# Kernel tuning notes

Measured on AMD Instinct MI355X. Metric: run time of the kernel, lower is better.

## Reference

```python
import jax, jax.numpy as jnp
import numpy as np

B, N, F, H, K, C = 2048, 62, 512, 128, 2, 2
EPS_BN = 1e-5
EPS_NORM = 1e-10
N_TRIL = N * (N + 1) // 2  # 1953, tril_indices incl. diagonal
FC_SIZES = [H * N, H * N // 2, H * N // 4, H * N // 8, C]  # [7936,3968,1984,992,2]


def setup_inputs() -> dict:
    key = jax.random.key(0)
    ks = jax.random.split(key, 16)
    inp = {
        "x": jax.random.normal(ks[0], (B, N, F), jnp.float32),
        "edge_weight": jax.random.uniform(ks[1], (N_TRIL,), jnp.float32),
        "bn_gamma": jnp.ones((F,), jnp.float32),
        "bn_beta": jnp.zeros((F,), jnp.float32),
        # xavier_normal for SGConv lin
        "lin_w": jax.random.normal(ks[2], (H, F), jnp.float32) * (2.0 / (F + H)) ** 0.5,
        "lin_b": jnp.zeros((H,), jnp.float32),
    }
    for i in range(4):
        fan_in, fan_out = FC_SIZES[i], FC_SIZES[i + 1]
        inp[f"fc{i}_w"] = jax.random.normal(ks[3 + i], (fan_out, fan_in), jnp.float32) * (2.0 / (fan_in + fan_out)) ** 0.5
        inp[f"fc{i}_b"] = jnp.zeros((fan_out,), jnp.float32)
    return inp


def _normalized_adj(edge_weight):
    """Build symmetric dense adjacency from tril params, normalize_matrix
    (relu + sym deg-norm), then SGConv.norm (D^-1/2 A D^-1/2; self-loops are
    already on the diagonal so add_remaining_self_loops is a no-op)."""
    xs, ys = np.tril_indices(N)
    Wm = jnp.zeros((N, N), jnp.float32).at[xs, ys].set(edge_weight)
    Wm = Wm + Wm.T - jnp.diag(jnp.diag(Wm))
    A = jax.nn.relu(Wm)
    dinv = jax.lax.rsqrt(A.sum(1) + EPS_NORM)
    A = dinv[:, None] * A * dinv[None, :]
    # SGConv normalization: deg = scatter_add over rows -> row sums
    deg = A.sum(1)
    dis = jnp.where(deg > 0, deg ** -0.5, 0.0)
    return dis[:, None] * A * dis[None, :]


def reference(x, edge_weight, bn_gamma, bn_beta, lin_w, lin_b,
              fc0_w, fc0_b, fc1_w, fc1_b, fc2_w, fc2_b, fc3_w, fc3_b):
    A = _normalized_adj(edge_weight)  # [N, N], shared across batch
    # BatchNorm1d over feature channels, stats over (batch, node) dims (train mode)
    mean = x.mean((0, 1))
    var = x.var((0, 1))
    h = (x - mean) * jax.lax.rsqrt(var + EPS_BN) * bn_gamma + bn_beta  # [B,N,F]
    # K-hop SGConv propagation == dense matmul with shared normalized adjacency
    for _ in range(K):
        h = jnp.einsum('ij,bjf->bif', A, h)
    h = h @ lin_w.T + lin_b           # [B, N, H]
    h = h.reshape(B, N * H)           # node-major flatten, matches x.view(batch,-1)
    # dropout is identity in eval mode
    for W, b in ((fc0_w, fc0_b), (fc1_w, fc1_b), (fc2_w, fc2_b)):
        h = jax.nn.relu(h @ W.T + b)
    return h @ fc3_w.T + fc3_b        # [B, C]
```

## Files before the change

kernel.cpp:

```cpp
#include <hip/hip_runtime.h>

typedef _Float16 f16;
typedef __attribute__((ext_vector_type(4))) _Float16 f16x4;
typedef __attribute__((ext_vector_type(8))) _Float16 f16x8;
typedef __attribute__((ext_vector_type(4))) float f32x4;

#define DEVI static __device__ __forceinline__

DEVI void async_copy16(const f16* g, f16* l) {
  __builtin_amdgcn_global_load_lds(
      (const __attribute__((address_space(1))) void*)g,
      (__attribute__((address_space(3))) void*)l, 16, 0, 0);
}

#define MEMPIN asm volatile("" ::: "memory")
#define RBAR __builtin_amdgcn_s_barrier()

__global__ __launch_bounds__(1024) void k_adj(const float* __restrict__ ew, float* __restrict__ out)
{
  __shared__ float sW[62][64];
  __shared__ float sT[62][64];
  __shared__ float d[62];
  const int tid = threadIdx.x;
  for (int idx = tid; idx < 62 * 62; idx += 1024) {
    int i = idx / 62, j = idx % 62;
    float w = (j <= i) ? ew[i * (i + 1) / 2 + j] : ew[j * (j + 1) / 2 + i];
    sW[i][j] = fmaxf(w, 0.f);
  }
  __syncthreads();
  if (tid < 62) {
    float s = 0.f;
    for (int j = 0; j < 62; j++) s += sW[tid][j];
    d[tid] = rsqrtf(s + 1e-10f);
  }
  __syncthreads();
  for (int idx = tid; idx < 62 * 62; idx += 1024) {
    int i = idx / 62, j = idx % 62;
    sW[i][j] *= d[i] * d[j];
  }
  __syncthreads();
  if (tid < 62) {
    float s = 0.f;
    for (int j = 0; j < 62; j++) s += sW[tid][j];
    d[tid] = (s > 0.f) ? rsqrtf(s) : 0.f;
  }
  __syncthreads();
  for (int idx = tid; idx < 62 * 62; idx += 1024) {
    int i = idx / 62, j = idx % 62;
    sW[i][j] *= d[i] * d[j];
  }
  __syncthreads();
  for (int idx = tid; idx < 62 * 64; idx += 1024) {
    int i = idx >> 6, j = idx & 63;
    float s = 0.f;
    if (j < 62) {
      for (int k = 0; k < 62; k++) s += sW[i][k] * sW[k][j];
    }
    sT[i][j] = s;
    out[idx] = s;
  }
  __syncthreads();
  if (tid < 62) {
    float s = 0.f;
    for (int j = 0; j < 62; j++) s += sT[tid][j];
    out[62 * 64 + tid] = s;
  }
}

__global__ __launch_bounds__(1024) void k_bnstats(const float* __restrict__ X, float* __restrict__ part)
{
  const int tid = threadIdx.x;
  const int c4 = (tid & 127) << 2;
  const int rg = tid >> 7;
  float sx = 0, sy = 0, sz = 0, sw = 0, qx = 0, qy = 0, qz = 0, qw = 0;
  const long r0 = (long)blockIdx.x * 496 + rg;
  for (int i = 0; i < 62; i++) {
    const float4 v = *(const float4*)(X + (r0 + 8 * i) * 512 + c4);
    sx += v.x; sy += v.y; sz += v.z; sw += v.w;
    qx += v.x * v.x; qy += v.y * v.y; qz += v.z * v.z; qw += v.w * v.w;
  }
  __shared__ float red[1024][8];
  red[tid][0] = sx; red[tid][1] = sy; red[tid][2] = sz; red[tid][3] = sw;
  red[tid][4] = qx; red[tid][5] = qy; red[tid][6] = qz; red[tid][7] = qw;
  __syncthreads();
  if (tid < 128) {
    float acc8[8];
#pragma unroll
    for (int j = 0; j < 8; j++) acc8[j] = 0.f;
#pragma unroll
    for (int g = 0; g < 8; g++)
#pragma unroll
      for (int j = 0; j < 8; j++) acc8[j] += red[g * 128 + tid][j];
    float* p = part + (long)blockIdx.x * 1024;
#pragma unroll
    for (int j = 0; j < 4; j++) p[c4 + j] = acc8[j];
#pragma unroll
    for (int j = 0; j < 4; j++) p[512 + c4 + j] = acc8[4 + j];
  }
}

__global__ __launch_bounds__(512) void k_bnfin(const float* __restrict__ part, const float* __restrict__ g,
                                               const float* __restrict__ be, float* __restrict__ ssb)
{
  const int c = threadIdx.x;
  float s = 0.f, q = 0.f;
  for (int b = 0; b < 256; b++) {
    s += part[b * 1024 + c];
    q += part[b * 1024 + 512 + c];
  }
  const float inv = 1.f / 126976.f;
  const float mean = s * inv;
  const float var = q * inv - mean * mean;
  const float sc = g[c] * rsqrtf(var + 1e-5f);
  ssb[c] = sc;
  ssb[512 + c] = be[c] - mean * sc;
}

__global__ __launch_bounds__(256) void k_foldw1(const float* __restrict__ lw, const float* __restrict__ ssb,
                                                f16* __restrict__ w1h, float* __restrict__ b1p)
{
  const int h = blockIdx.x;
  const int tid = threadIdx.x;
  float partl = 0.f;
  for (int f = tid; f < 512; f += 256) {
    const float w = lw[h * 512 + f];
    w1h[h * 512 + f] = (f16)(w * ssb[f]);
    partl += w * ssb[512 + f];
  }
  __shared__ float red[256];
  red[tid] = partl;
  __syncthreads();
  for (int s = 128; s; s >>= 1) {
    if (tid < s) red[tid] += red[tid + s];
    __syncthreads();
  }
  if (tid == 0) b1p[h] = red[0];
}

__global__ __launch_bounds__(256) void k_cvtw(const float* __restrict__ src, f16* __restrict__ dst,
                                              int N, int K, int Npad, int Kpad)
{
  const long total4 = (long)Npad * Kpad / 4;
  const int kp4 = Kpad >> 2;
  for (long i = (long)blockIdx.x * 256 + threadIdx.x; i < total4; i += (long)gridDim.x * 256) {
    const long n = i / kp4;
    const int k = (int)(i % kp4) << 2;
    f16x4 h;
    if (n < N && k < K) {
      const float4 v = *(const float4*)(src + n * K + k);
      h[0] = (f16)v.x; h[1] = (f16)v.y; h[2] = (f16)v.z; h[3] = (f16)v.w;
    } else {
      h[0] = (f16)0.f; h[1] = (f16)0.f; h[2] = (f16)0.f; h[3] = (f16)0.f;
    }
    *(f16x4*)(dst + i * 4) = h;
  }
}

__global__ __launch_bounds__(256, 2) void k_linprop(
    const float* __restrict__ X, const f16* __restrict__ Bw,
    const float* __restrict__ A2, const float* __restrict__ b1p,
    const float* __restrict__ lb, f16* __restrict__ Z)
{
  __shared__ f16 smem[128 * 128];
  __shared__ float sA2[62 * 64];
  __shared__ float sR[62];
  __shared__ float sB1[128];
  __shared__ float sLB[128];
  f16* sA = smem;
  f16* sB = smem + 8192;
  const int tid = threadIdx.x;
  const int lane = tid & 63;
  const int wave = tid >> 6;
  const int wr = wave >> 1, wc = wave & 1;
  const long rowA0 = (long)blockIdx.x * 124;

  for (int i = tid; i < 992; i += 256)
    *(float4*)&sA2[i * 4] = *(const float4*)(A2 + i * 4);
  if (tid < 62) sR[tid] = A2[3968 + tid];
  if (tid < 128) sB1[tid] = b1p[tid];
  if (tid >= 128) sLB[tid - 128] = lb[tid - 128];

  const int srow = tid >> 3;
  const int scolb = (tid & 7) << 4;
  const int gcolb = scolb ^ ((srow & 7) << 4);
  const f16* gB = Bw + (long)srow * 512 + (gcolb >> 1);
  f16* lB = sB + srow * 64 + (scolb >> 1);

  const int ac4 = tid & 15;
  const int ar0 = tid >> 4;
  const int aswz = (ar0 & 7) << 4;
  char* lAbase = (char*)sA + ar0 * 128 + ((ac4 * 8) ^ aswz);

  const int frow = lane & 15;
  const int kb = (lane >> 4) << 4;
  const int rswz = (lane & 7) << 4;

  f32x4 acc[4][4] = {};

  for (int kt = 0; kt < 512; kt += 64) {
#pragma unroll
    for (int i = 0; i < 8; i++) {
      long rr = rowA0 + ar0 + 16 * i;
      if (rr > 126975) rr = 126975;
      const float4 v = *(const float4*)(X + rr * 512 + kt + ac4 * 4);
      f16x4 hh;
      hh[0] = (f16)v.x; hh[1] = (f16)v.y; hh[2] = (f16)v.z; hh[3] = (f16)v.w;
      *(f16x4*)(lAbase + 16 * i * 128) = hh;
    }
#pragma unroll
    for (int i = 0; i < 4; i++)
      async_copy16(gB + kt + (long)i * (32 * 512), lB + i * 2048);
    __syncthreads();
#pragma unroll
    for (int kk = 0; kk < 2; kk++) {
      f16x8 af[4], bf[4];
#pragma unroll
      for (int m = 0; m < 4; m++) {
        const int row = wr * 64 + m * 16 + frow;
        af[m] = *(const f16x8*)((const char*)sA + row * 128 + ((kk * 64 + kb) ^ rswz));
      }
#pragma unroll
      for (int n = 0; n < 4; n++) {
        const int row = wc * 64 + n * 16 + frow;
        bf[n] = *(const f16x8*)((const char*)sB + row * 128 + ((kk * 64 + kb) ^ rswz));
      }
#pragma unroll
      for (int m = 0; m < 4; m++)
#pragma unroll
        for (int n = 0; n < 4; n++)
          acc[m][n] = __builtin_amdgcn_mfma_f32_16x16x32_f16(af[m], bf[n], acc[m][n], 0, 0, 0);
    }
    __syncthreads();
  }

  const int crow = wr * 64 + ((lane >> 4) << 2);
  const int ccol = wc * 64 + (lane & 15);
#pragma unroll
  for (int n = 0; n < 4; n++)
#pragma unroll
    for (int m = 0; m < 4; m++)
#pragma unroll
      for (int r = 0; r < 4; r++)
        smem[(crow + m * 16 + r) * 128 + ccol + n * 16] = (f16)acc[m][n][r];
  __syncthreads();

  const int h = tid & 127;
  const int g = tid >> 7;
  float yc[62];
#pragma unroll
  for (int j = 0; j < 62; j++) yc[j] = (float)smem[(g * 62 + j) * 128 + h];
  const float bh1 = sB1[h];
  const float bh2 = sLB[h];
  f16* zp = Z + ((long)blockIdx.x * 2 + g) * 7936 + h;
  for (int n = 0; n < 62; n++) {
    float s = 0.f;
#pragma unroll
    for (int j = 0; j < 62; j++) s += sA2[n * 64 + j] * yc[j];
    zp[n * 128] = (f16)(s + sR[n] * bh1 + bh2);
  }
}

template <int LOOPN, int MT, int NT, int KS>
__global__ __launch_bounds__(512, 2) void k_fc8(
    const f16* __restrict__ A, const f16* __restrict__ Bw, f16* __restrict__ P,
    const int K, const int kslice, const int PLD)
{
  __shared__ f16 sA[2][256 * 64];
  __shared__ f16 sB[2][256 * 64];
  const int tid = threadIdx.x;
  const int bid = blockIdx.x;
  const int xcd = bid & 7, ii = bid >> 3;
  int nt, mt, ks;
  if constexpr (NT == 16) {
    nt = xcd * 2 + (ii & 1); mt = (ii >> 1) & (MT - 1); ks = ii >> 4;
  } else {
    nt = xcd; mt = ii & (MT - 1); ks = ii >> 3;
  }
  const long rowA0 = (long)mt * 256;
  const long rowB0 = (long)nt * 256;
  const long k0 = (long)ks * kslice;

  const int srow = tid >> 3;
  const int scolb = (tid & 7) << 4;
  const int gcolb = scolb ^ ((srow & 7) << 4);
  const f16* gA = A + (rowA0 + srow) * (long)K + k0 + (gcolb >> 1);
  const f16* gB = Bw + (rowB0 + srow) * (long)K + k0 + (gcolb >> 1);

#define SGA(d, q, kt) async_copy16(gA + (kt) + (long)(q) * 64 * K, &sA[d][0] + (q) * 4096 + tid * 8)
#define SGB(d, q, kt) async_copy16(gB + (kt) + (long)(q) * 64 * K, &sB[d][0] + (q) * 4096 + tid * 8)

  const int lane = tid & 63;
  const int wave = tid >> 6;
  const int wr = wave >> 2;
  const int wc = wave & 3;
  const int frow = lane & 15;
  const int kb = (lane >> 4) << 4;
  const int rsw = (frow & 7) << 4;

  f32x4 acc[8][4] = {};
  f16x8 af[4][2], bf[4][2];

#define RDA(d, mh) do { _Pragma("unroll") for (int m_ = 0; m_ < 4; m_++) {                      \
    const int row_ = wr * 128 + (mh) * 64 + m_ * 16 + frow;                                     \
    af[m_][0] = *(const f16x8*)((const char*)&sA[d][0] + row_ * 128 + (kb ^ rsw));              \
    af[m_][1] = *(const f16x8*)((const char*)&sA[d][0] + row_ * 128 + ((64 + kb) ^ rsw)); } } while (0)
#define RDB(d) do { _Pragma("unroll") for (int n_ = 0; n_ < 4; n_++) {                          \
    const int row_ = wc * 64 + n_ * 16 + frow;                                                  \
    bf[n_][0] = *(const f16x8*)((const char*)&sB[d][0] + row_ * 128 + (kb ^ rsw));              \
    bf[n_][1] = *(const f16x8*)((const char*)&sB[d][0] + row_ * 128 + ((64 + kb) ^ rsw)); } } while (0)
#define QUAD(mh, nh) do { _Pragma("unroll") for (int m_ = 0; m_ < 4; m_++)                      \
    _Pragma("unroll") for (int n_ = 0; n_ < 2; n_++) {                                          \
      acc[(mh)*4+m_][(nh)*2+n_] = __builtin_amdgcn_mfma_f32_16x16x32_f16(af[m_][0], bf[(nh)*2+n_][0], acc[(mh)*4+m_][(nh)*2+n_], 0, 0, 0); \
      acc[(mh)*4+m_][(nh)*2+n_] = __builtin_amdgcn_mfma_f32_16x16x32_f16(af[m_][1], bf[(nh)*2+n_][1], acc[(mh)*4+m_][(nh)*2+n_], 0, 0, 0); } } while (0)
#define VMW8 asm volatile("s_waitcnt vmcnt(8)" ::: "memory")
#define VMW0 asm volatile("s_waitcnt vmcnt(0)" ::: "memory")
#define PRIO1 __builtin_amdgcn_s_setprio(1)
#define PRIO0 __builtin_amdgcn_s_setprio(0)

  SGA(0, 0, 0); SGA(0, 2, 0); SGB(0, 0, 0); SGB(0, 1, 0);
  SGA(0, 1, 0); SGA(0, 3, 0); SGB(0, 2, 0); SGB(0, 3, 0);
  SGA(1, 0, 64); SGA(1, 2, 64); SGB(1, 0, 64); SGB(1, 1, 64);
  SGA(1, 1, 64); SGA(1, 3, 64); SGB(1, 2, 64); SGB(1, 3, 64);

  for (int t = 0; t < LOOPN; ++t) {
    const long kt2 = (long)(t + 1) * 128;
    VMW8; MEMPIN; RBAR; MEMPIN;
    RDA(0, 0); RDB(0);
    PRIO1; QUAD(0, 0); PRIO0;
    MEMPIN; RBAR; MEMPIN;
    SGA(0, 0, kt2); SGA(0, 2, kt2); SGB(0, 0, kt2); SGB(0, 1, kt2);
    QUAD(0, 1);
    RDA(0, 1);
    QUAD(1, 0);
    MEMPIN; RBAR; MEMPIN;
    SGA(0, 1, kt2); SGA(0, 3, kt2); SGB(0, 2, kt2); SGB(0, 3, kt2);
    QUAD(1, 1);
    VMW8; MEMPIN; RBAR; MEMPIN;
    RDA(1, 0); RDB(1);
    PRIO1; QUAD(0, 0); PRIO0;
    MEMPIN; RBAR; MEMPIN;
    SGA(1, 0, kt2 + 64); SGA(1, 2, kt2 + 64); SGB(1, 0, kt2 + 64); SGB(1, 1, kt2 + 64);
    QUAD(0, 1);
    RDA(1, 1);
    QUAD(1, 0);
    MEMPIN; RBAR; MEMPIN;
    SGA(1, 1, kt2 + 64); SGA(1, 3, kt2 + 64); SGB(1, 2, kt2 + 64); SGB(1, 3, kt2 + 64);
    QUAD(1, 1);
  }
  VMW8; MEMPIN; RBAR; MEMPIN;
  RDA(0, 0); RDB(0);
  PRIO1; QUAD(0, 0); QUAD(0, 1); PRIO0;
  RDA(0, 1);
  PRIO1; QUAD(1, 0); QUAD(1, 1); PRIO0;
  VMW0; MEMPIN; RBAR; MEMPIN;
  RDA(1, 0); RDB(1);
  PRIO1; QUAD(0, 0); QUAD(0, 1); PRIO0;
  RDA(1, 1);
  PRIO1; QUAD(1, 0); QUAD(1, 1); PRIO0;

  f16* Pp = P + (long)ks * 2048 * PLD;
#pragma unroll
  for (int mi = 0; mi < 8; mi++) {
    const long r0 = rowA0 + wr * 128 + (mi >> 2) * 64 + (mi & 3) * 16 + ((lane >> 4) << 2);
#pragma unroll
    for (int n = 0; n < 4; n++) {
      const long col = rowB0 + wc * 64 + n * 16 + (lane & 15);
#pragma unroll
      for (int r = 0; r < 4; r++)
        Pp[(r0 + r) * PLD + col] = (f16)acc[mi][n][r];
    }
  }
#undef SGA
#undef SGB
#undef RDA
#undef RDB
#undef QUAD
#undef VMW8
#undef VMW0
#undef PRIO1
#undef PRIO0
}

template <int S>
__global__ __launch_bounds__(256) void k_fixs(const f16* __restrict__ P, const float* __restrict__ b,
                                              f16* __restrict__ C, int N, int realN)
{
  const long total = 2048L * N;
  const int mask = N - 1;
  const long stride = (long)gridDim.x * 256 * 8;
  for (long i = ((long)blockIdx.x * 256 + threadIdx.x) * 8; i < total; i += stride) {
    float s[8];
#pragma unroll
    for (int j = 0; j < 8; j++) s[j] = 0.f;
#pragma unroll
    for (int ps = 0; ps < S; ps++) {
      const f16x8 p = *(const f16x8*)(P + (long)ps * total + i);
#pragma unroll
      for (int j = 0; j < 8; j++) s[j] += (float)p[j];
    }
    const int col = (int)(i & mask);
    f16x8 o;
#pragma unroll
    for (int j = 0; j < 8; j++) {
      const int c = col + j;
      const float bb = (c < realN) ? b[c] : 0.f;
      o[j] = (f16)fmaxf(s[j] + bb, 0.f);
    }
    *(f16x8*)(C + i) = o;
  }
}

template <int RELU>
__global__ __launch_bounds__(256, 2) void k_gemm_f16(
    const f16* __restrict__ A, const f16* __restrict__ B,
    const float* __restrict__ bias, f16* __restrict__ C,
    int N, int K, int realN)
{
  __shared__ f16 sA[128 * 64];
  __shared__ f16 sB[128 * 64];
  const int tid = threadIdx.x;
  const int lane = tid & 63;
  const int wave = tid >> 6;
  const int wr = wave >> 1, wc = wave & 1;
  const int bid = blockIdx.x;
  const int xcd = bid & 7, idx = bid >> 3;
  const long rowA0 = (long)(xcd * 2 + (idx & 1)) * 128;
  const long rowB0 = (long)(idx >> 1) * 128;

  const int srow = tid >> 3;
  const int scolb = (tid & 7) << 4;
  const int gcolb = scolb ^ ((srow & 7) << 4);
  const f16* gA = A + (rowA0 + srow) * (long)K + (gcolb >> 1);
  const f16* gB = B + (rowB0 + srow) * (long)K + (gcolb >> 1);
  f16* lA = sA + srow * 64 + (scolb >> 1);
  f16* lB = sB + srow * 64 + (scolb >> 1);
  const long rstep = 32L * K;

  const int frow = lane & 15;
  const int kb = (lane >> 4) << 4;
  const int rswz = (lane & 7) << 4;

  f32x4 acc[4][4] = {};

  for (int kt = 0; kt < K; kt += 64) {
#pragma unroll
    for (int i = 0; i < 4; i++) {
      async_copy16(gA + kt + i * rstep, lA + i * 2048);
      async_copy16(gB + kt + i * rstep, lB + i * 2048);
    }
    __syncthreads();
#pragma unroll
    for (int kk = 0; kk < 2; kk++) {
      f16x8 af[4], bf[4];
#pragma unroll
      for (int m = 0; m < 4; m++) {
        const int row = wr * 64 + m * 16 + frow;
        af[m] = *(const f16x8*)((const char*)sA + row * 128 + ((kk * 64 + kb) ^ rswz));
      }
#pragma unroll
      for (int n = 0; n < 4; n++) {
        const int row = wc * 64 + n * 16 + frow;
        bf[n] = *(const f16x8*)((const char*)sB + row * 128 + ((kk * 64 + kb) ^ rswz));
      }
#pragma unroll
      for (int m = 0; m < 4; m++)
#pragma unroll
        for (int n = 0; n < 4; n++)
          acc[m][n] = __builtin_amdgcn_mfma_f32_16x16x32_f16(af[m], bf[n], acc[m][n], 0, 0, 0);
    }
    __syncthreads();
  }

  const int crow = wr * 64 + ((lane >> 4) << 2);
  const int ccol = wc * 64 + (lane & 15);
#pragma unroll
  for (int n = 0; n < 4; n++) {
    const int col = (int)rowB0 + ccol + n * 16;
    const float bb = (col < realN) ? bias[col] : 0.f;
#pragma unroll
    for (int m = 0; m < 4; m++) {
      const long gr = rowA0 + crow + m * 16;
#pragma unroll
      for (int r = 0; r < 4; r++) {
        float v = acc[m][n][r] + bb;
        if (RELU) v = fmaxf(v, 0.f);
        C[(gr + r) * N + col] = (f16)v;
      }
    }
  }
}

__global__ __launch_bounds__(256) void k_fc3(const f16* __restrict__ H, const float* __restrict__ W,
                                             const float* __restrict__ b, float* __restrict__ out)
{
  const int row = blockIdx.x * 4 + (threadIdx.x >> 6);
  const int lane = threadIdx.x & 63;
  const f16* h = H + (long)row * 1024;
  float a0 = 0.f, a1 = 0.f;
  for (int k = lane; k < 992; k += 64) {
    const float v = (float)h[k];
    a0 += v * W[k];
    a1 += v * W[992 + k];
  }
  for (int off = 32; off; off >>= 1) {
    a0 += __shfl_down(a0, off);
    a1 += __shfl_down(a1, off);
  }
  if (lane == 0) {
    out[row * 2 + 0] = a0 + b[0];
    out[row * 2 + 1] = a1 + b[1];
  }
}

extern "C" void kernel_launch(void* const* d_in, const int* in_sizes, int n_in,
                              void* d_out, int out_size, void* d_ws, size_t ws_size,
                              hipStream_t stream)
{
  const float* x    = (const float*)d_in[0];
  const float* ew   = (const float*)d_in[1];
  const float* bng  = (const float*)d_in[2];
  const float* bnb  = (const float*)d_in[3];
  const float* linw = (const float*)d_in[4];
  const float* linb = (const float*)d_in[5];
  const float* w0   = (const float*)d_in[6];
  const float* b0   = (const float*)d_in[7];
  const float* w1   = (const float*)d_in[8];
  const float* b1   = (const float*)d_in[9];
  const float* w2   = (const float*)d_in[10];
  const float* b2   = (const float*)d_in[11];
  const float* w3   = (const float*)d_in[12];
  const float* b3   = (const float*)d_in[13];
  float* out = (float*)d_out;
  char* ws = (char*)d_ws;

  constexpr size_t oA2  = 0;
  constexpr size_t oSS  = 16384;
  constexpr size_t oB1P = 20480;
  constexpr size_t oW1H = 20992;
  constexpr size_t oP   = 152064;
  constexpr size_t oACC = oP;
  constexpr size_t oZ   = 33706496;
  constexpr size_t oW0H = 66212352;
  constexpr size_t WS_NEED = 131224064;
  constexpr size_t oH0  = oZ;
  constexpr size_t oW1F = oZ + 16777216;
  constexpr size_t oH1  = 67260928;
  constexpr size_t oW2F = 75649536;
  constexpr size_t oH2  = 79843840;
  if (ws_size < WS_NEED) return;

  float* A2  = (float*)(ws + oA2);
  float* acc = (float*)(ws + oACC);
  float* ssb = (float*)(ws + oSS);
  float* b1p = (float*)(ws + oB1P);
  f16* w1h = (f16*)(ws + oW1H);
  f16* P   = (f16*)(ws + oP);
  f16* Z   = (f16*)(ws + oZ);
  f16* w0h = (f16*)(ws + oW0H);
  f16* h0  = (f16*)(ws + oH0);
  f16* w1f = (f16*)(ws + oW1F);
  f16* h1  = (f16*)(ws + oH1);
  f16* w2f = (f16*)(ws + oW2F);
  f16* h2  = (f16*)(ws + oH2);

  k_adj<<<1, 1024, 0, stream>>>(ew, A2);
  k_bnstats<<<256, 1024, 0, stream>>>(x, acc);
  k_bnfin<<<1, 512, 0, stream>>>(acc, bng, bnb, ssb);
  k_foldw1<<<128, 256, 0, stream>>>(linw, ssb, w1h, b1p);
  k_cvtw<<<1024, 256, 0, stream>>>(w0, w0h, 3968, 7936, 4096, 7936);
  k_linprop<<<1024, 256, 0, stream>>>(x, w1h, A2, b1p, linb, Z);
  k_fc8<30, 8, 16, 2><<<256, 512, 0, stream>>>(Z, w0h, P, 7936, 3968, 4096);
  k_fixs<2><<<2048, 256, 0, stream>>>(P, b0, h0, 4096, 3968);
  k_cvtw<<<512, 256, 0, stream>>>(w1, w1f, 1984, 3968, 2048, 4096);
  k_cvtw<<<256, 256, 0, stream>>>(w2, w2f, 992, 1984, 1024, 2048);
  k_fc8<7, 8, 8, 4><<<256, 512, 0, stream>>>(h0, w1f, P, 4096, 1024, 2048);
  k_fixs<4><<<1024, 256, 0, stream>>>(P, b1, h1, 2048, 1984);
  k_gemm_f16<1><<<128, 256, 0, stream>>>(h1, w2f, b2, h2, 1024, 2048, 992);
  k_fc3<<<512, 256, 0, stream>>>(h2, w3, b3, out);
}
```

Measured before the change: 475.2 us.

## Restructure GEMM main loop into eight-phase interleaved load/MFMA schedule

Reworks the double-buffered fp16 GEMM inner loop into eight phases. Each phase pairs a partial LDS fragment read (A halves, and B now split into halves) and two async global-to-LDS copies with one MFMA quadrant, fenced by barriers. The prologue preloads fewer stages and waits at vmcnt(6) instead of 8. The aim is finer interleaving of memory traffic with matrix math, in the style of a ping-pong schedule. The cost is many more workgroup barriers per iteration, with the risk of stalls or LDS read/write hazards if the fencing is wrong.

```diff
diff --git a/kernel.cpp b/kernel.cpp
--- a/kernel.cpp
+++ b/kernel.cpp
@@ -298,65 +298,72 @@
   const int rsw = (frow & 7) << 4;
 
   f32x4 acc[8][4] = {};
-  f16x8 af[4][2], bf[4][2];
+  f16x8 af[4][2];
+  f16x8 bf[4][2];
 
 #define RDA(d, mh) do { _Pragma("unroll") for (int m_ = 0; m_ < 4; m_++) {                      \
     const int row_ = wr * 128 + (mh) * 64 + m_ * 16 + frow;                                     \
     af[m_][0] = *(const f16x8*)((const char*)&sA[d][0] + row_ * 128 + (kb ^ rsw));              \
     af[m_][1] = *(const f16x8*)((const char*)&sA[d][0] + row_ * 128 + ((64 + kb) ^ rsw)); } } while (0)
-#define RDB(d) do { _Pragma("unroll") for (int n_ = 0; n_ < 4; n_++) {                          \
-    const int row_ = wc * 64 + n_ * 16 + frow;                                                  \
-    bf[n_][0] = *(const f16x8*)((const char*)&sB[d][0] + row_ * 128 + (kb ^ rsw));              \
-    bf[n_][1] = *(const f16x8*)((const char*)&sB[d][0] + row_ * 128 + ((64 + kb) ^ rsw)); } } while (0)
+#define RDBH(d, nh) do { _Pragma("unroll") for (int n_ = 0; n_ < 2; n_++) {                     \
+    const int row_ = wc * 64 + (nh) * 32 + n_ * 16 + frow;                                      \
+    bf[(nh)*2+n_][0] = *(const f16x8*)((const char*)&sB[d][0] + row_ * 128 + (kb ^ rsw));       \
+    bf[(nh)*2+n_][1] = *(const f16x8*)((const char*)&sB[d][0] + row_ * 128 + ((64 + kb) ^ rsw)); } } while (0)
 #define QUAD(mh, nh) do { _Pragma("unroll") for (int m_ = 0; m_ < 4; m_++)                      \
     _Pragma("unroll") for (int n_ = 0; n_ < 2; n_++) {                                          \
       acc[(mh)*4+m_][(nh)*2+n_] = __builtin_amdgcn_mfma_f32_16x16x32_f16(af[m_][0], bf[(nh)*2+n_][0], acc[(mh)*4+m_][(nh)*2+n_], 0, 0, 0); \
       acc[(mh)*4+m_][(nh)*2+n_] = __builtin_amdgcn_mfma_f32_16x16x32_f16(af[m_][1], bf[(nh)*2+n_][1], acc[(mh)*4+m_][(nh)*2+n_], 0, 0, 0); } } while (0)
-#define VMW8 asm volatile("s_waitcnt vmcnt(8)" ::: "memory")
+#define VMW6 asm volatile("s_waitcnt vmcnt(6)" ::: "memory")
 #define VMW0 asm volatile("s_waitcnt vmcnt(0)" ::: "memory")
 #define PRIO1 __builtin_amdgcn_s_setprio(1)
 #define PRIO0 __builtin_amdgcn_s_setprio(0)
+#define BAR1 do { MEMPIN; RBAR; MEMPIN; } while (0)
 
   SGA(0, 0, 0); SGA(0, 2, 0); SGB(0, 0, 0); SGB(0, 1, 0);
-  SGA(0, 1, 0); SGA(0, 3, 0); SGB(0, 2, 0); SGB(0, 3, 0);
+  SGB(0, 2, 0); SGB(0, 3, 0); SGA(0, 1, 0); SGA(0, 3, 0);
   SGA(1, 0, 64); SGA(1, 2, 64); SGB(1, 0, 64); SGB(1, 1, 64);
-  SGA(1, 1, 64); SGA(1, 3, 64); SGB(1, 2, 64); SGB(1, 3, 64);
+  SGB(1, 2, 64); SGB(1, 3, 64);
+  VMW6; BAR1;
 
   for (int t = 0; t < LOOPN; ++t) {
-    const long kt2 = (long)(t + 1) * 128;
-    VMW8; MEMPIN; RBAR; MEMPIN;
-    RDA(0, 0); RDB(0);
+    const long ktD1 = (long)t * 128 + 64;
+    const long ktN  = (long)(t + 1) * 128;
+    const long ktN1 = ktN + 64;
+    RDA(0, 0); RDBH(0, 0); SGA(1, 1, ktD1); SGA(1, 3, ktD1);
+    BAR1; PRIO1; QUAD(0, 0); PRIO0; BAR1;
+    RDBH(0, 1); SGA(0, 0, ktN); SGA(0, 2, ktN);
+    BAR1; PRIO1; QUAD(0, 1); PRIO0; BAR1;
+    RDA(0, 1); SGB(0, 0, ktN); SGB(0, 1, ktN);
+    BAR1; PRIO1; QUAD(1, 0); PRIO0; BAR1;
+    SGB(0, 2, ktN); SGB(0, 3, ktN);
+    BAR1; PRIO1; QUAD(1, 1); PRIO0; VMW6; BAR1;
+    RDA(1, 0); RDBH(1, 0); SGA(0, 1, ktN); SGA(0, 3, ktN);
+    BAR1; PRIO1; QUAD(0, 0); PRIO0; BAR1;
+    RDBH(1, 1); SGA(1, 0, ktN1); SGA(1, 2, ktN1);
+    BAR1; PRIO1; QUAD(0, 1); PRIO0; BAR1;
+    RDA(1, 1); SGB(1, 0, ktN1); SGB(1, 1, ktN1);
+    BAR1; PRIO1; QUAD(1, 0); PRIO0; BAR1;
+    SGB(1, 2, ktN1); SGB(1, 3, ktN1);
+    BAR1; PRIO1; QUAD(1, 1); PRIO0; VMW6; BAR1;
+  }
+
+  {
+    const long ktD1 = (long)LOOPN * 128 + 64;
+    RDA(0, 0); RDBH(0, 0); SGA(1, 1, ktD1); SGA(1, 3, ktD1);
+    BAR1; PRIO1; QUAD(0, 0); PRIO0; BAR1;
+    RDBH(0, 1);
+    BAR1; PRIO1; QUAD(0, 1); PRIO0; BAR1;
+    RDA(0, 1);
+    BAR1; PRIO1; QUAD(1, 0); PRIO0; BAR1;
+    PRIO1; QUAD(1, 1); PRIO0; VMW0; BAR1;
+    RDA(1, 0); RDBH(1, 0);
     PRIO1; QUAD(0, 0); PRIO0;
-    MEMPIN; RBAR; MEMPIN;
-    SGA(0, 0, kt2); SGA(0, 2, kt2); SGB(0, 0, kt2); SGB(0, 1, kt2);
-    QUAD(0, 1);
-    RDA(0, 1);
-    QUAD(1, 0);
-    MEMPIN; RBAR; MEMPIN;
-    SGA(0, 1, kt2); SGA(0, 3, kt2); SGB(0, 2, kt2); SGB(0, 3, kt2);
-    QUAD(1, 1);
-    VMW8; MEMPIN; RBAR; MEMPIN;
-    RDA(1, 0); RDB(1);
-    PRIO1; QUAD(0, 0); PRIO0;
-    MEMPIN; RBAR; MEMPIN;
-    SGA(1, 0, kt2 + 64); SGA(1, 2, kt2 + 64); SGB(1, 0, kt2 + 64); SGB(1, 1, kt2 + 64);
-    QUAD(0, 1);
+    RDBH(1, 1);
+    PRIO1; QUAD(0, 1); PRIO0;
     RDA(1, 1);
-    QUAD(1, 0);
-    MEMPIN; RBAR; MEMPIN;
-    SGA(1, 1, kt2 + 64); SGA(1, 3, kt2 + 64); SGB(1, 2, kt2 + 64); SGB(1, 3, kt2 + 64);
-    QUAD(1, 1);
-  }
-  VMW8; MEMPIN; RBAR; MEMPIN;
-  RDA(0, 0); RDB(0);
-  PRIO1; QUAD(0, 0); QUAD(0, 1); PRIO0;
-  RDA(0, 1);
-  PRIO1; QUAD(1, 0); QUAD(1, 1); PRIO0;
-  VMW0; MEMPIN; RBAR; MEMPIN;
-  RDA(1, 0); RDB(1);
-  PRIO1; QUAD(0, 0); QUAD(0, 1); PRIO0;
-  RDA(1, 1);
-  PRIO1; QUAD(1, 0); QUAD(1, 1); PRIO0;
+    PRIO1; QUAD(1, 0); PRIO0;
+    PRIO1; QUAD(1, 1); PRIO0;
+  }
 
   f16* Pp = P + (long)ks * 2048 * PLD;
 #pragma unroll
@@ -373,12 +380,13 @@
 #undef SGA
 #undef SGB
 #undef RDA
-#undef RDB
+#undef RDBH
 #undef QUAD
-#undef VMW8
+#undef VMW6
 #undef VMW0
 #undef PRIO1
 #undef PRIO0
+#undef BAR1
 }
 
 template <int S>
```

New measurement: 492.0 us. 1.04x slower.
